# Performance work log

Measured on AMD Instinct MI355X. Metric: run time of the kernel, lower is better.

The kernel has to match this reference:

```python
import jax, jax.numpy as jnp
import numpy as np

CLIP_DIM = 1024
X_DIM = 768
NUM_HEADS = 8
HEAD_DIM = X_DIM // NUM_HEADS
SCALE = HEAD_DIM ** -0.5
EPS1 = 1e-6  # custom channel-first LayerNorm
EPS2 = 1e-5  # nn.LayerNorm default


def setup_inputs() -> dict:
    key = jax.random.key(0)
    ks = jax.random.split(key, 12)
    B, H, W = 8, 32, 32
    d = X_DIM
    inp = {
        "x": jax.random.normal(ks[0], (B, H, W, d), jnp.float32),
        "clip_features": jax.random.normal(ks[1], (B, CLIP_DIM, 16, 16), jnp.float32),
        "conv_w": jax.random.normal(ks[2], (CLIP_DIM, d), jnp.float32) * (CLIP_DIM ** -0.5),
        "conv_b": jnp.zeros((d,), jnp.float32),
        "ln1_w": jnp.ones((d,), jnp.float32),
        "ln1_b": jnp.zeros((d,), jnp.float32),
        "wq": jax.random.normal(ks[3], (d, d), jnp.float32) * (d ** -0.5),
        "bq": jnp.zeros((d,), jnp.float32),
        "wk": jax.random.normal(ks[4], (d, d), jnp.float32) * (d ** -0.5),
        "bk": jnp.zeros((d,), jnp.float32),
        "wv": jax.random.normal(ks[5], (d, d), jnp.float32) * (d ** -0.5),
        "bv": jnp.zeros((d,), jnp.float32),
        "wo": jax.random.normal(ks[6], (d, d), jnp.float32) * (d ** -0.5),
        "bo": jnp.zeros((d,), jnp.float32),
        "ln2_w": jnp.ones((d,), jnp.float32),
        "ln2_b": jnp.zeros((d,), jnp.float32),
    }
    return inp


def _forward(x, clip_features, conv_w, conv_b, ln1_w, ln1_b,
             wq, bq, wk, bk, wv, bv, wo, bo, ln2_w, ln2_b):
    B, H, W, d = x.shape
    S = H * W
    # bilinear resize (align_corners=False == half-pixel, jax default)
    clip_r = jax.image.resize(clip_features, (B, CLIP_DIM, H, W), method="bilinear")
    # 1x1 conv: bchw,cd->bdhw
    c = jnp.einsum("bchw,cd->bdhw", clip_r, conv_w) + conv_b[None, :, None, None]
    # channel-first LayerNorm over dim 1
    u = c.mean(1, keepdims=True)
    s = ((c - u) ** 2).mean(1, keepdims=True)
    c = (c - u) * jax.lax.rsqrt(s + EPS1)
    c = ln1_w[None, :, None, None] * c + ln1_b[None, :, None, None]
    # to (B, S, d)
    q_in = jnp.transpose(c, (0, 2, 3, 1)).reshape(B, S, d)
    kv_in = x.reshape(B, S, d)
    # projections -> (B, h, S, hd)
    def heads(t):
        return jnp.transpose(t.reshape(B, S, NUM_HEADS, HEAD_DIM), (0, 2, 1, 3))
    q = heads(q_in @ wq + bq)
    k = heads(kv_in @ wk + bk)
    v = heads(kv_in @ wv + bv)
    scores = jnp.einsum("bhqd,bhkd->bhqk", q, k) * SCALE
    attn = jax.nn.softmax(scores, axis=-1)
    o = jnp.einsum("bhqk,bhkd->bhqd", attn, v)
    o = jnp.transpose(o, (0, 2, 1, 3)).reshape(B, S, d)
    o = o @ wo + bo
    # standard LayerNorm over last dim
    mu = o.mean(-1, keepdims=True)
    var = ((o - mu) ** 2).mean(-1, keepdims=True)
    o = (o - mu) * jax.lax.rsqrt(var + EPS2) * ln2_w + ln2_b
    return o.reshape(B, H, W, d)


def reference(x, clip_features, conv_w, conv_b, ln1_w, ln1_b,
              wq, bq, wk, bk, wv, bv, wo, bo, ln2_w, ln2_b):
    return _forward(x, clip_features, conv_w, conv_b, ln1_w, ln1_b,
                    wq, bq, wk, bk, wv, bv, wo, bo, ln2_w, ln2_b)
```

## Files before the change

kernel.cpp:

```cpp
#include <hip/hip_runtime.h>
#include <hip/hip_bf16.h>

typedef __attribute__((ext_vector_type(8))) short short8;
typedef __attribute__((ext_vector_type(4))) short short4v;
typedef __attribute__((ext_vector_type(4))) float floatx4;
typedef unsigned short u16;

__device__ __forceinline__ float b2f(u16 u) {
    unsigned int x = ((unsigned int)u) << 16;
    float f;
    __builtin_memcpy(&f, &x, 4);
    return f;
}
__device__ __forceinline__ u16 f2b(float f) {
    unsigned int x;
    __builtin_memcpy(&x, &f, 4);
    unsigned int lsb = (x >> 16) & 1u;
    x += 0x7fffu + lsb;
    return (u16)(x >> 16);
}

__device__ __forceinline__ void gload16(const u16* g, u16* l) {
    __builtin_amdgcn_global_load_lds(
        (const __attribute__((address_space(1))) void*)g,
        (__attribute__((address_space(3))) void*)l,
        16, 0, 0);
}

__global__ __launch_bounds__(256) void transpose_all(const float* __restrict__ clip,
                                                     const float* __restrict__ conv_w,
                                                     const float* __restrict__ w0,
                                                     const float* __restrict__ w1,
                                                     const float* __restrict__ w2,
                                                     const float* __restrict__ w3,
                                                     const float* __restrict__ x,
                                                     u16* __restrict__ clipT,
                                                     u16* __restrict__ convwT,
                                                     u16* __restrict__ wT,
                                                     u16* __restrict__ xb) {
    int id = blockIdx.x;
    if (id >= 5120) {
        int i = (id - 5120) * 256 + threadIdx.x;
        float4 f0 = ((const float4*)x)[i * 2];
        float4 f1 = ((const float4*)x)[i * 2 + 1];
        short8 s;
        s[0] = (short)f2b(f0.x); s[1] = (short)f2b(f0.y);
        s[2] = (short)f2b(f0.z); s[3] = (short)f2b(f0.w);
        s[4] = (short)f2b(f1.x); s[5] = (short)f2b(f1.y);
        s[6] = (short)f2b(f1.z); s[7] = (short)f2b(f1.w);
        ((short8*)xb)[i] = s;
        return;
    }
    __shared__ float tile[32][33];
    const float* ip;
    u16* op;
    int R, C, c0, r0;
    if (id < 2048) {
        int b = id >> 8, rem = id & 255;
        R = 1024; C = 256;
        c0 = (rem & 7) * 32; r0 = (rem >> 3) * 32;
        ip = clip + (long)b * 262144;
        op = clipT + (long)b * 262144;
    } else if (id < 2816) {
        int i2 = id - 2048;
        R = 1024; C = 768;
        c0 = (i2 % 24) * 32; r0 = (i2 / 24) * 32;
        ip = conv_w;
        op = convwT;
    } else {
        int i3 = id - 2816;
        int z = i3 / 576, rem = i3 % 576;
        R = 768; C = 768;
        c0 = (rem % 24) * 32; r0 = (rem / 24) * 32;
        ip = (z == 0) ? w0 : (z == 1) ? w1 : (z == 2) ? w2 : w3;
        op = wT + (long)z * 589824;
    }
    int tx = threadIdx.x & 31, ty = threadIdx.x >> 5;
    for (int j = 0; j < 32; j += 8)
        tile[ty + j][tx] = ip[(long)(r0 + ty + j) * C + c0 + tx];
    __syncthreads();
    for (int j = 0; j < 32; j += 8)
        op[(long)(c0 + ty + j) * R + r0 + tx] = f2b(tile[tx][ty + j]);
}

__global__ __launch_bounds__(256) void gemm_ld64(const u16* __restrict__ A,
                                                 const u16* __restrict__ Bt,
                                                 const float* __restrict__ bias,
                                                 u16* __restrict__ Cv,
                                                 int M, int N, int K, int ldc,
                                                 float oscale) {
    __shared__ __align__(16) u16 lA[128 * 64];
    __shared__ __align__(16) u16 lB[64 * 64];
    int tid = threadIdx.x, lane = tid & 63, w = tid >> 6;
    int m0 = blockIdx.x * 128, n0 = blockIdx.y * 64;
    floatx4 acc[2][4] = {};
    const int lr = lane & 15, kg = lane >> 4;
    int rt = tid >> 3, sl = ((tid & 7) ^ (rt & 7)) * 8;
    const u16* gA0 = &A[(long)(m0 + rt) * K + sl];
    const u16* gA1 = &A[(long)(m0 + 32 + rt) * K + sl];
    const u16* gA2 = &A[(long)(m0 + 64 + rt) * K + sl];
    const u16* gA3 = &A[(long)(m0 + 96 + rt) * K + sl];
    const u16* gB0 = &Bt[(long)(n0 + rt) * K + sl];
    const u16* gB1 = &Bt[(long)(n0 + 32 + rt) * K + sl];
    const int s0 = (kg ^ (lr & 7)) * 8;
    for (int k0 = 0; k0 < K; k0 += 64) {
        gload16(gA0 + k0, &lA[w * 512]);
        gload16(gA1 + k0, &lA[2048 + w * 512]);
        gload16(gA2 + k0, &lA[4096 + w * 512]);
        gload16(gA3 + k0, &lA[6144 + w * 512]);
        gload16(gB0 + k0, &lB[w * 512]);
        gload16(gB1 + k0, &lB[2048 + w * 512]);
        __syncthreads();
        #pragma unroll
        for (int ks = 0; ks < 2; ks++) {
            int sseg = s0 ^ (ks << 5);
            short8 a0 = *(const short8*)&lA[(w * 32 + lr) * 64 + sseg];
            short8 a1 = *(const short8*)&lA[(w * 32 + 16 + lr) * 64 + sseg];
            #pragma unroll
            for (int ni = 0; ni < 4; ni++) {
                short8 bf = *(const short8*)&lB[(ni * 16 + lr) * 64 + sseg];
                acc[0][ni] = __builtin_amdgcn_mfma_f32_16x16x32_bf16(a0, bf, acc[0][ni], 0, 0, 0);
                acc[1][ni] = __builtin_amdgcn_mfma_f32_16x16x32_bf16(a1, bf, acc[1][ni], 0, 0, 0);
            }
        }
        __syncthreads();
    }
    #pragma unroll
    for (int mi = 0; mi < 2; mi++)
        #pragma unroll
        for (int ni = 0; ni < 4; ni++) {
            int n = n0 + ni * 16 + lr;
            float bv = bias[n];
            #pragma unroll
            for (int r = 0; r < 4; r++) {
                int m = m0 + w * 32 + mi * 16 + kg * 4 + r;
                Cv[(long)m * ldc + n] = f2b((acc[mi][ni][r] + bv) * oscale);
            }
        }
}

__global__ __launch_bounds__(256) void gemm128kv(const u16* __restrict__ A,
                                                 const u16* __restrict__ Bt,
                                                 const float* __restrict__ biasA,
                                                 const float* __restrict__ biasB,
                                                 u16* __restrict__ Cv,
                                                 u16* __restrict__ vTout,
                                                 int M, int N, int K, int ldc) {
    __shared__ __align__(16) u16 lA[128 * 64];
    __shared__ __align__(16) u16 lB[128 * 64];
    int tid = threadIdx.x, lane = tid & 63, w = tid >> 6;
    int wr = w >> 1, wc = w & 1;
    int m0 = blockIdx.x * 128, n0 = blockIdx.y * 128;
    floatx4 acc[4][4] = {};
    const int lr = lane & 15, kg = lane >> 4;
    int rt = tid >> 3, sl = ((tid & 7) ^ (rt & 7)) * 8;
    const u16* gA0 = &A[(long)(m0 + rt) * K + sl];
    const u16* gA1 = &A[(long)(m0 + 32 + rt) * K + sl];
    const u16* gA2 = &A[(long)(m0 + 64 + rt) * K + sl];
    const u16* gA3 = &A[(long)(m0 + 96 + rt) * K + sl];
    const u16* gB0 = &Bt[(long)(n0 + rt) * K + sl];
    const u16* gB1 = &Bt[(long)(n0 + 32 + rt) * K + sl];
    const u16* gB2 = &Bt[(long)(n0 + 64 + rt) * K + sl];
    const u16* gB3 = &Bt[(long)(n0 + 96 + rt) * K + sl];
    const int s0 = (kg ^ (lr & 7)) * 8;
    for (int k0 = 0; k0 < K; k0 += 64) {
        gload16(gA0 + k0, &lA[w * 512]);
        gload16(gA1 + k0, &lA[2048 + w * 512]);
        gload16(gA2 + k0, &lA[4096 + w * 512]);
        gload16(gA3 + k0, &lA[6144 + w * 512]);
        gload16(gB0 + k0, &lB[w * 512]);
        gload16(gB1 + k0, &lB[2048 + w * 512]);
        gload16(gB2 + k0, &lB[4096 + w * 512]);
        gload16(gB3 + k0, &lB[6144 + w * 512]);
        __syncthreads();
        #pragma unroll
        for (int ks = 0; ks < 2; ks++) {
            int sseg = s0 ^ (ks << 5);
            short8 af[4], bf[4];
            #pragma unroll
            for (int mi = 0; mi < 4; mi++)
                af[mi] = *(const short8*)&lA[(wr * 64 + mi * 16 + lr) * 64 + sseg];
            #pragma unroll
            for (int ni = 0; ni < 4; ni++)
                bf[ni] = *(const short8*)&lB[(wc * 64 + ni * 16 + lr) * 64 + sseg];
            #pragma unroll
            for (int mi = 0; mi < 4; mi++)
                #pragma unroll
                for (int ni = 0; ni < 4; ni++)
                    acc[mi][ni] = __builtin_amdgcn_mfma_f32_16x16x32_bf16(af[mi], bf[ni], acc[mi][ni], 0, 0, 0);
        }
        __syncthreads();
    }
    #pragma unroll
    for (int mi = 0; mi < 4; mi++)
        #pragma unroll
        for (int ni = 0; ni < 4; ni++) {
            int n = n0 + wc * 64 + ni * 16 + lr;
            float bv = (n < 768) ? biasA[n] : biasB[n - 768];
            if (n >= 768) {
                int fg = n - 768;
                int h = fg / 96, f = fg - h * 96;
                int mb = m0 + wr * 64 + mi * 16 + kg * 4;
                long vrow = ((long)((m0 >> 10) * 8 + h) * 96 + f) * 1024 + (mb & 1023);
                short4v pk;
                #pragma unroll
                for (int r = 0; r < 4; r++) pk[r] = (short)f2b(acc[mi][ni][r] + bv);
                *(short4v*)&vTout[vrow] = pk;
            } else {
                #pragma unroll
                for (int r = 0; r < 4; r++) {
                    int m = m0 + wr * 64 + mi * 16 + kg * 4 + r;
                    Cv[(long)m * ldc + n] = f2b(acc[mi][ni][r] + bv);
                }
            }
        }
}

__global__ __launch_bounds__(256) void ln1_resize_w(const u16* __restrict__ t_lo,
                                                    const float* __restrict__ lnw,
                                                    const float* __restrict__ lnb,
                                                    u16* __restrict__ q_in) {
    int wv = threadIdx.x >> 6, lane = threadIdx.x & 63;
    int b = blockIdx.z, oh = blockIdx.y, ow = blockIdx.x * 4 + wv;
    float sy = oh * 0.5f - 0.25f;
    int iy = (int)floorf(sy);
    float fy = sy - (float)iy;
    int y0 = min(max(iy, 0), 15), y1 = min(max(iy + 1, 0), 15);
    float sx = ow * 0.5f - 0.25f;
    int ix = (int)floorf(sx);
    float fx = sx - (float)ix;
    int x0 = min(max(ix, 0), 15), x1 = min(max(ix + 1, 0), 15);
    float w00 = (1.f - fy) * (1.f - fx), w01 = (1.f - fy) * fx;
    float w10 = fy * (1.f - fx), w11 = fy * fx;
    long base = (long)b * 256 * 768;
    long i00 = base + (long)(y0 * 16 + x0) * 768;
    long i01 = base + (long)(y0 * 16 + x1) * 768;
    long i10 = base + (long)(y1 * 16 + x0) * 768;
    long i11 = base + (long)(y1 * 16 + x1) * 768;
    float v[12];
    float s = 0.f, sq = 0.f;
    #pragma unroll
    for (int j = 0; j < 3; j++) {
        int c0 = (j * 64 + lane) * 4;
        short4v a = *(const short4v*)&t_lo[i00 + c0];
        short4v c = *(const short4v*)&t_lo[i01 + c0];
        short4v d = *(const short4v*)&t_lo[i10 + c0];
        short4v e = *(const short4v*)&t_lo[i11 + c0];
        #pragma unroll
        for (int k = 0; k < 4; k++) {
            float val = w00 * b2f((u16)a[k]) + w01 * b2f((u16)c[k]) +
                        w10 * b2f((u16)d[k]) + w11 * b2f((u16)e[k]);
            v[j * 4 + k] = val;
            s += val;
            sq += val * val;
        }
    }
    #pragma unroll
    for (int off = 32; off >= 1; off >>= 1) {
        s += __shfl_xor(s, off);
        sq += __shfl_xor(sq, off);
    }
    float mean = s * (1.f / 768.f);
    float var = sq * (1.f / 768.f) - mean * mean;
    float rstd = rsqrtf(var + 1e-6f);
    long orow = ((long)b * 1024 + oh * 32 + ow) * 768;
    #pragma unroll
    for (int j = 0; j < 3; j++) {
        int c0 = (j * 64 + lane) * 4;
        float4 w4 = *(const float4*)&lnw[c0];
        float4 b4 = *(const float4*)&lnb[c0];
        short4v o;
        o[0] = (short)f2b((v[j * 4 + 0] - mean) * rstd * w4.x + b4.x);
        o[1] = (short)f2b((v[j * 4 + 1] - mean) * rstd * w4.y + b4.y);
        o[2] = (short)f2b((v[j * 4 + 2] - mean) * rstd * w4.z + b4.z);
        o[3] = (short)f2b((v[j * 4 + 3] - mean) * rstd * w4.w + b4.w);
        *(short4v*)&q_in[orow + c0] = o;
    }
}

#define PP 76
__global__ __launch_bounds__(512) void attn_kernel(const u16* __restrict__ Q,
                                                   const u16* __restrict__ Km,
                                                   const u16* __restrict__ Vt,
                                                   u16* __restrict__ O) {
    __shared__ __align__(16) u16 lK[2 * 4096];
    __shared__ __align__(16) u16 lKb[2 * 2048];
    __shared__ __align__(16) u16 lV[2 * 6144];
    __shared__ __align__(16) u16 lP[128 * PP];
    int tid = threadIdx.x, lane = tid & 63, w = tid >> 6;
    int L = blockIdx.x + (blockIdx.y << 3) + (blockIdx.z << 6);
    int b = L & 7, h = (L >> 3) & 7, qt = L >> 6;
    const int lr = lane & 15, kg = lane >> 4;

    long qrow = ((long)b * 1024 + qt * 128 + w * 16 + lr) * 768 + h * 96;
    short8 aq[3];
    for (int ks = 0; ks < 3; ks++) aq[ks] = *(const short8*)&Q[qrow + ks * 32 + kg * 8];

    floatx4 acco[6] = {};
    float lrun[4] = {0.f, 0.f, 0.f, 0.f};

    long kvbase = ((long)b * 1024) * 768 + h * 96;
    long vtbase = ((long)(b * 8 + h)) * 96 * 1024;

    const u16* gp[3];
    u16* lp[3];
    int gs[3], bs[3];
    #pragma unroll
    for (int i = 0; i < 3; i++) {
        int id = tid + i * 512;
        if (id < 512) {
            int row = id >> 3, lg = (id & 7) ^ (row & 7);
            lp[i] = &lK[id * 8];
            gp[i] = &Km[kvbase + (long)row * 768 + lg * 8];
            gs[i] = 64 * 768;
            bs[i] = 4096;
        } else if (id < 768) {
            int j = id - 512;
            int row = j >> 2, lg = (j & 3) ^ (row & 3);
            lp[i] = &lKb[j * 8];
            gp[i] = &Km[kvbase + (long)row * 768 + 64 + lg * 8];
            gs[i] = 64 * 768;
            bs[i] = 2048;
        } else {
            int j = id - 768;
            int f = j >> 3, lg = (j & 7) ^ (f & 7);
            lp[i] = &lV[j * 8];
            gp[i] = &Vt[vtbase + (long)f * 1024 + lg * 8];
            gs[i] = 64;
            bs[i] = 6144;
        }
    }

    const int sA = (kg ^ (lr & 7)) * 8;
    const int sB = (kg ^ (lr & 3)) * 8;

    #pragma unroll
    for (int i = 0; i < 3; i++) {
        gload16(gp[i], lp[i]);
        gp[i] += gs[i];
    }

    for (int kt = 0; kt < 16; kt++) {
        int cur = kt & 1, nxt = cur ^ 1;
        if (kt < 15) {
            #pragma unroll
            for (int i = 0; i < 3; i++) {
                gload16(gp[i], lp[i] + nxt * bs[i]);
                gp[i] += gs[i];
            }
            asm volatile("s_waitcnt vmcnt(3)" ::: "memory");
        } else {
            asm volatile("s_waitcnt vmcnt(0)" ::: "memory");
        }
        __builtin_amdgcn_sched_barrier(0);
        __builtin_amdgcn_s_barrier();

        const u16* K0 = &lK[cur * 4096];
        const u16* Kb0 = &lKb[cur * 2048];
        const u16* V0 = &lV[cur * 6144];

        floatx4 accs[4] = {};
        __builtin_amdgcn_s_setprio(1);
        for (int ni = 0; ni < 4; ni++) {
            int rb = (ni * 16 + lr);
            short8 bk0 = *(const short8*)&K0[rb * 64 + sA];
            short8 bk1 = *(const short8*)&K0[rb * 64 + (sA ^ 32)];
            short8 bk2 = *(const short8*)&Kb0[rb * 32 + sB];
            accs[ni] = __builtin_amdgcn_mfma_f32_16x16x32_bf16(aq[0], bk0, accs[ni], 0, 0, 0);
            accs[ni] = __builtin_amdgcn_mfma_f32_16x16x32_bf16(aq[1], bk1, accs[ni], 0, 0, 0);
            accs[ni] = __builtin_amdgcn_mfma_f32_16x16x32_bf16(aq[2], bk2, accs[ni], 0, 0, 0);
        }
        __builtin_amdgcn_s_setprio(0);

        for (int r = 0; r < 4; r++) {
            float p0 = __builtin_amdgcn_exp2f(accs[0][r]);
            float p1 = __builtin_amdgcn_exp2f(accs[1][r]);
            float p2 = __builtin_amdgcn_exp2f(accs[2][r]);
            float p3 = __builtin_amdgcn_exp2f(accs[3][r]);
            lrun[r] += (p0 + p1) + (p2 + p3);
            int prow = w * 16 + kg * 4 + r;
            lP[prow * PP + 0 + lr] = f2b(p0);
            lP[prow * PP + 16 + lr] = f2b(p1);
            lP[prow * PP + 32 + lr] = f2b(p2);
            lP[prow * PP + 48 + lr] = f2b(p3);
        }

        short8 ap0 = *(const short8*)&lP[(w * 16 + lr) * PP + kg * 8];
        short8 ap1 = *(const short8*)&lP[(w * 16 + lr) * PP + 32 + kg * 8];
        __builtin_amdgcn_s_setprio(1);
        for (int nb = 0; nb < 6; nb++) {
            int fb = (nb * 16 + lr);
            short8 bv0 = *(const short8*)&V0[fb * 64 + sA];
            short8 bv1 = *(const short8*)&V0[fb * 64 + (sA ^ 32)];
            acco[nb] = __builtin_amdgcn_mfma_f32_16x16x32_bf16(ap0, bv0, acco[nb], 0, 0, 0);
            acco[nb] = __builtin_amdgcn_mfma_f32_16x16x32_bf16(ap1, bv1, acco[nb], 0, 0, 0);
        }
        __builtin_amdgcn_s_setprio(0);
        __builtin_amdgcn_s_barrier();
    }

    #pragma unroll
    for (int r = 0; r < 4; r++)
        for (int off = 1; off < 16; off <<= 1) lrun[r] += __shfl_xor(lrun[r], off);
    float invl[4];
    #pragma unroll
    for (int r = 0; r < 4; r++) invl[r] = 1.0f / lrun[r];

    long obase = ((long)b * 1024 + qt * 128 + w * 16) * 768 + h * 96;
    for (int nb = 0; nb < 6; nb++)
        for (int r = 0; r < 4; r++) {
            float val = acco[nb][r] * invl[r];
            O[obase + (long)(kg * 4 + r) * 768 + nb * 16 + lr] = f2b(val);
        }
}

__global__ __launch_bounds__(256) void ln2_w(const u16* __restrict__ o,
                                             const float* __restrict__ lnw,
                                             const float* __restrict__ lnb,
                                             float* __restrict__ out) {
    int wv = threadIdx.x >> 6, lane = threadIdx.x & 63;
    long row = (long)blockIdx.x * 4 + wv;
    long base = row * 768;
    float v[12];
    float s = 0.f, sq = 0.f;
    #pragma unroll
    for (int j = 0; j < 3; j++) {
        int c0 = (j * 64 + lane) * 4;
        short4v a = *(const short4v*)&o[base + c0];
        #pragma unroll
        for (int k = 0; k < 4; k++) {
            float val = b2f((u16)a[k]);
            v[j * 4 + k] = val;
            s += val;
            sq += val * val;
        }
    }
    #pragma unroll
    for (int off = 32; off >= 1; off >>= 1) {
        s += __shfl_xor(s, off);
        sq += __shfl_xor(sq, off);
    }
    float mean = s * (1.f / 768.f);
    float var = sq * (1.f / 768.f) - mean * mean;
    float rstd = rsqrtf(var + 1e-5f);
    #pragma unroll
    for (int j = 0; j < 3; j++) {
        int c0 = (j * 64 + lane) * 4;
        float4 w4 = *(const float4*)&lnw[c0];
        float4 b4 = *(const float4*)&lnb[c0];
        float4 r4;
        r4.x = (v[j * 4 + 0] - mean) * rstd * w4.x + b4.x;
        r4.y = (v[j * 4 + 1] - mean) * rstd * w4.y + b4.y;
        r4.z = (v[j * 4 + 2] - mean) * rstd * w4.z + b4.z;
        r4.w = (v[j * 4 + 3] - mean) * rstd * w4.w + b4.w;
        *(float4*)&out[base + c0] = r4;
    }
}

extern "C" void kernel_launch(void* const* d_in, const int* in_sizes, int n_in,
                              void* d_out, int out_size, void* d_ws, size_t ws_size,
                              hipStream_t stream) {
    const float* x       = (const float*)d_in[0];
    const float* clip    = (const float*)d_in[1];
    const float* conv_w  = (const float*)d_in[2];
    const float* conv_b  = (const float*)d_in[3];
    const float* ln1_w   = (const float*)d_in[4];
    const float* ln1_b   = (const float*)d_in[5];
    const float* wq      = (const float*)d_in[6];
    const float* bq      = (const float*)d_in[7];
    const float* wk      = (const float*)d_in[8];
    const float* bk      = (const float*)d_in[9];
    const float* wv      = (const float*)d_in[10];
    const float* bv      = (const float*)d_in[11];
    const float* wo      = (const float*)d_in[12];
    const float* bo      = (const float*)d_in[13];
    const float* ln2_w_  = (const float*)d_in[14];
    const float* ln2_b_  = (const float*)d_in[15];
    float* out = (float*)d_out;

    u16* ws = (u16*)d_ws;
    u16* clipT   = ws;
    u16* convwT  = clipT + 2097152;
    u16* wqT     = convwT + 786432;
    u16* wkT     = wqT + 589824;
    u16* wvT     = wkT + 589824;
    u16* woT     = wvT + 589824;
    u16* t_lo    = woT + 589824;
    u16* q_in    = t_lo + 1572864;
    u16* qb      = q_in + 6291456;
    u16* kb      = qb + 6291456;
    u16* vT      = kb + 6291456;
    u16* xb      = vT + 6291456;
    u16* attno   = q_in;
    u16* obuf    = qb;

    const float QSCALE = 0.10206207261596575f * 1.4426950408889634f;

    transpose_all<<<8192, 256, 0, stream>>>(clip, conv_w, wq, wk, wv, wo, x,
                                            clipT, convwT, wqT, xb);

    gemm_ld64<<<dim3(16, 12), 256, 0, stream>>>(clipT, convwT, conv_b, t_lo,
                                                2048, 768, 1024, 768, 1.0f);

    ln1_resize_w<<<dim3(8, 32, 8), 256, 0, stream>>>(t_lo, ln1_w, ln1_b, q_in);

    gemm_ld64<<<dim3(64, 12), 256, 0, stream>>>(q_in, wqT, bq, qb, 8192, 768, 768, 768, QSCALE);

    gemm128kv<<<dim3(64, 12), 256, 0, stream>>>(xb, wkT, bk, bv, kb, vT, 8192, 1536, 768, 768);

    attn_kernel<<<dim3(8, 8, 8), 512, 0, stream>>>(qb, kb, vT, attno);

    gemm_ld64<<<dim3(64, 12), 256, 0, stream>>>(attno, woT, bo, obuf, 8192, 768, 768, 768, 1.0f);

    ln2_w<<<2048, 256, 0, stream>>>(obuf, ln2_w_, ln2_b_, out);
}
```

Before: 136.7 us.

## Merge conv GEMM and KV projection GEMM into one launch

Folds the small 1x1-conv GEMM (192 tiles, 2048x768x1024) and the K/V projection GEMM (768 tiles) into one kernel with 960 blocks, dispatched by block index. The conv GEMM on its own launches too few blocks to fill the GPU, and merging lets it run alongside the larger independent GEMM while also removing one launch. The trade-off is a heterogeneous grid in which conv blocks do longer K loops with smaller tiles, which can leave a load-imbalanced tail.

```diff
diff --git a/kernel.cpp b/kernel.cpp
--- a/kernel.cpp
+++ b/kernel.cpp
@@ -139,81 +139,133 @@
         }
 }
 
-__global__ __launch_bounds__(256) void gemm128kv(const u16* __restrict__ A,
-                                                 const u16* __restrict__ Bt,
-                                                 const float* __restrict__ biasA,
-                                                 const float* __restrict__ biasB,
-                                                 u16* __restrict__ Cv,
-                                                 u16* __restrict__ vTout,
-                                                 int M, int N, int K, int ldc) {
+__global__ __launch_bounds__(256) void gemm_convkv(const u16* __restrict__ xb,
+                                                   const u16* __restrict__ wkvT,
+                                                   const float* __restrict__ bk,
+                                                   const float* __restrict__ bv,
+                                                   u16* __restrict__ kb,
+                                                   u16* __restrict__ vTout,
+                                                   const u16* __restrict__ clipT,
+                                                   const u16* __restrict__ convwT,
+                                                   const float* __restrict__ conv_b,
+                                                   u16* __restrict__ t_lo) {
     __shared__ __align__(16) u16 lA[128 * 64];
     __shared__ __align__(16) u16 lB[128 * 64];
     int tid = threadIdx.x, lane = tid & 63, w = tid >> 6;
-    int wr = w >> 1, wc = w & 1;
-    int m0 = blockIdx.x * 128, n0 = blockIdx.y * 128;
-    floatx4 acc[4][4] = {};
     const int lr = lane & 15, kg = lane >> 4;
     int rt = tid >> 3, sl = ((tid & 7) ^ (rt & 7)) * 8;
-    const u16* gA0 = &A[(long)(m0 + rt) * K + sl];
-    const u16* gA1 = &A[(long)(m0 + 32 + rt) * K + sl];
-    const u16* gA2 = &A[(long)(m0 + 64 + rt) * K + sl];
-    const u16* gA3 = &A[(long)(m0 + 96 + rt) * K + sl];
-    const u16* gB0 = &Bt[(long)(n0 + rt) * K + sl];
-    const u16* gB1 = &Bt[(long)(n0 + 32 + rt) * K + sl];
-    const u16* gB2 = &Bt[(long)(n0 + 64 + rt) * K + sl];
-    const u16* gB3 = &Bt[(long)(n0 + 96 + rt) * K + sl];
     const int s0 = (kg ^ (lr & 7)) * 8;
-    for (int k0 = 0; k0 < K; k0 += 64) {
-        gload16(gA0 + k0, &lA[w * 512]);
-        gload16(gA1 + k0, &lA[2048 + w * 512]);
-        gload16(gA2 + k0, &lA[4096 + w * 512]);
-        gload16(gA3 + k0, &lA[6144 + w * 512]);
-        gload16(gB0 + k0, &lB[w * 512]);
-        gload16(gB1 + k0, &lB[2048 + w * 512]);
-        gload16(gB2 + k0, &lB[4096 + w * 512]);
-        gload16(gB3 + k0, &lB[6144 + w * 512]);
-        __syncthreads();
-        #pragma unroll
-        for (int ks = 0; ks < 2; ks++) {
-            int sseg = s0 ^ (ks << 5);
-            short8 af[4], bf[4];
-            #pragma unroll
-            for (int mi = 0; mi < 4; mi++)
-                af[mi] = *(const short8*)&lA[(wr * 64 + mi * 16 + lr) * 64 + sseg];
-            #pragma unroll
-            for (int ni = 0; ni < 4; ni++)
-                bf[ni] = *(const short8*)&lB[(wc * 64 + ni * 16 + lr) * 64 + sseg];
-            #pragma unroll
-            for (int mi = 0; mi < 4; mi++)
+    int id = blockIdx.x;
+    if (id < 768) {
+        const int K = 768;
+        int wr = w >> 1, wc = w & 1;
+        int m0 = (id & 63) * 128, n0 = (id >> 6) * 128;
+        floatx4 acc[4][4] = {};
+        const u16* gA0 = &xb[(long)(m0 + rt) * K + sl];
+        const u16* gA1 = &xb[(long)(m0 + 32 + rt) * K + sl];
+        const u16* gA2 = &xb[(long)(m0 + 64 + rt) * K + sl];
+        const u16* gA3 = &xb[(long)(m0 + 96 + rt) * K + sl];
+        const u16* gB0 = &wkvT[(long)(n0 + rt) * K + sl];
+        const u16* gB1 = &wkvT[(long)(n0 + 32 + rt) * K + sl];
+        const u16* gB2 = &wkvT[(long)(n0 + 64 + rt) * K + sl];
+        const u16* gB3 = &wkvT[(long)(n0 + 96 + rt) * K + sl];
+        for (int k0 = 0; k0 < K; k0 += 64) {
+            gload16(gA0 + k0, &lA[w * 512]);
+            gload16(gA1 + k0, &lA[2048 + w * 512]);
+            gload16(gA2 + k0, &lA[4096 + w * 512]);
+            gload16(gA3 + k0, &lA[6144 + w * 512]);
+            gload16(gB0 + k0, &lB[w * 512]);
+            gload16(gB1 + k0, &lB[2048 + w * 512]);
+            gload16(gB2 + k0, &lB[4096 + w * 512]);
+            gload16(gB3 + k0, &lB[6144 + w * 512]);
+            __syncthreads();
+            #pragma unroll
+            for (int ks = 0; ks < 2; ks++) {
+                int sseg = s0 ^ (ks << 5);
+                short8 af[4], bf[4];
+                #pragma unroll
+                for (int mi = 0; mi < 4; mi++)
+                    af[mi] = *(const short8*)&lA[(wr * 64 + mi * 16 + lr) * 64 + sseg];
                 #pragma unroll
                 for (int ni = 0; ni < 4; ni++)
-                    acc[mi][ni] = __builtin_amdgcn_mfma_f32_16x16x32_bf16(af[mi], bf[ni], acc[mi][ni], 0, 0, 0);
-        }
-        __syncthreads();
-    }
-    #pragma unroll
-    for (int mi = 0; mi < 4; mi++)
+                    bf[ni] = *(const short8*)&lB[(wc * 64 + ni * 16 + lr) * 64 + sseg];
+                #pragma unroll
+                for (int mi = 0; mi < 4; mi++)
+                    #pragma unroll
+                    for (int ni = 0; ni < 4; ni++)
+                        acc[mi][ni] = __builtin_amdgcn_mfma_f32_16x16x32_bf16(af[mi], bf[ni], acc[mi][ni], 0, 0, 0);
+            }
+            __syncthreads();
+        }
         #pragma unroll
-        for (int ni = 0; ni < 4; ni++) {
-            int n = n0 + wc * 64 + ni * 16 + lr;
-            float bv = (n < 768) ? biasA[n] : biasB[n - 768];
-            if (n >= 768) {
-                int fg = n - 768;
-                int h = fg / 96, f = fg - h * 96;
-                int mb = m0 + wr * 64 + mi * 16 + kg * 4;
-                long vrow = ((long)((m0 >> 10) * 8 + h) * 96 + f) * 1024 + (mb & 1023);
-                short4v pk;
+        for (int mi = 0; mi < 4; mi++)
+            #pragma unroll
+            for (int ni = 0; ni < 4; ni++) {
+                int n = n0 + wc * 64 + ni * 16 + lr;
+                float bvv = (n < 768) ? bk[n] : bv[n - 768];
+                if (n >= 768) {
+                    int fg = n - 768;
+                    int h = fg / 96, f = fg - h * 96;
+                    int mb = m0 + wr * 64 + mi * 16 + kg * 4;
+                    long vrow = ((long)((m0 >> 10) * 8 + h) * 96 + f) * 1024 + (mb & 1023);
+                    short4v pk;
+                    #pragma unroll
+                    for (int r = 0; r < 4; r++) pk[r] = (short)f2b(acc[mi][ni][r] + bvv);
+                    *(short4v*)&vTout[vrow] = pk;
+                } else {
+                    #pragma unroll
+                    for (int r = 0; r < 4; r++) {
+                        int m = m0 + wr * 64 + mi * 16 + kg * 4 + r;
+                        kb[(long)m * 768 + n] = f2b(acc[mi][ni][r] + bvv);
+                    }
+                }
+            }
+    } else {
+        const int K = 1024;
+        int id2 = id - 768;
+        int m0 = (id2 & 15) * 128, n0 = (id2 >> 4) * 64;
+        floatx4 acc[2][4] = {};
+        const u16* gA0 = &clipT[(long)(m0 + rt) * K + sl];
+        const u16* gA1 = &clipT[(long)(m0 + 32 + rt) * K + sl];
+        const u16* gA2 = &clipT[(long)(m0 + 64 + rt) * K + sl];
+        const u16* gA3 = &clipT[(long)(m0 + 96 + rt) * K + sl];
+        const u16* gB0 = &convwT[(long)(n0 + rt) * K + sl];
+        const u16* gB1 = &convwT[(long)(n0 + 32 + rt) * K + sl];
+        for (int k0 = 0; k0 < K; k0 += 64) {
+            gload16(gA0 + k0, &lA[w * 512]);
+            gload16(gA1 + k0, &lA[2048 + w * 512]);
+            gload16(gA2 + k0, &lA[4096 + w * 512]);
+            gload16(gA3 + k0, &lA[6144 + w * 512]);
+            gload16(gB0 + k0, &lB[w * 512]);
+            gload16(gB1 + k0, &lB[2048 + w * 512]);
+            __syncthreads();
+            #pragma unroll
+            for (int ks = 0; ks < 2; ks++) {
+                int sseg = s0 ^ (ks << 5);
+                short8 a0 = *(const short8*)&lA[(w * 32 + lr) * 64 + sseg];
+                short8 a1 = *(const short8*)&lA[(w * 32 + 16 + lr) * 64 + sseg];
                 #pragma unroll
-                for (int r = 0; r < 4; r++) pk[r] = (short)f2b(acc[mi][ni][r] + bv);
-                *(short4v*)&vTout[vrow] = pk;
-            } else {
+                for (int ni = 0; ni < 4; ni++) {
+                    short8 bf = *(const short8*)&lB[(ni * 16 + lr) * 64 + sseg];
+                    acc[0][ni] = __builtin_amdgcn_mfma_f32_16x16x32_bf16(a0, bf, acc[0][ni], 0, 0, 0);
+                    acc[1][ni] = __builtin_amdgcn_mfma_f32_16x16x32_bf16(a1, bf, acc[1][ni], 0, 0, 0);
+                }
+            }
+            __syncthreads();
+        }
+        #pragma unroll
+        for (int mi = 0; mi < 2; mi++)
+            #pragma unroll
+            for (int ni = 0; ni < 4; ni++) {
+                int n = n0 + ni * 16 + lr;
+                float bvv = conv_b[n];
                 #pragma unroll
                 for (int r = 0; r < 4; r++) {
-                    int m = m0 + wr * 64 + mi * 16 + kg * 4 + r;
-                    Cv[(long)m * ldc + n] = f2b(acc[mi][ni][r] + bv);
+                    int m = m0 + w * 32 + mi * 16 + kg * 4 + r;
+                    t_lo[(long)m * 768 + n] = f2b(acc[mi][ni][r] + bvv);
                 }
             }
-        }
+    }
 }
 
 __global__ __launch_bounds__(256) void ln1_resize_w(const u16* __restrict__ t_lo,
@@ -499,15 +551,13 @@
     transpose_all<<<8192, 256, 0, stream>>>(clip, conv_w, wq, wk, wv, wo, x,
                                             clipT, convwT, wqT, xb);
 
-    gemm_ld64<<<dim3(16, 12), 256, 0, stream>>>(clipT, convwT, conv_b, t_lo,
-                                                2048, 768, 1024, 768, 1.0f);
+    gemm_convkv<<<960, 256, 0, stream>>>(xb, wkT, bk, bv, kb, vT,
+                                         clipT, convwT, conv_b, t_lo);
 
     ln1_resize_w<<<dim3(8, 32, 8), 256, 0, stream>>>(t_lo, ln1_w, ln1_b, q_in);
 
     gemm_ld64<<<dim3(64, 12), 256, 0, stream>>>(q_in, wqT, bq, qb, 8192, 768, 768, 768, QSCALE);
 
-    gemm128kv<<<dim3(64, 12), 256, 0, stream>>>(xb, wkT, bk, bv, kb, vT, 8192, 1536, 768, 768);
-
     attn_kernel<<<dim3(8, 8, 8), 512, 0, stream>>>(qb, kb, vT, attno);
 
     gemm_ld64<<<dim3(64, 12), 256, 0, stream>>>(attno, woT, bo, obuf, 8192, 768, 768, 768, 1.0f);
```

Measured after the change: 130.6 us. 4.4% less time.
